# Performance work log

Hardware: AMD Instinct MI355X
Metric: run time of the kernel (lower is better)

The kernel has to match this reference:

```python
import jax, jax.numpy as jnp
import numpy as np

N, DIM, G, K = 100000, 512, 4, 16
GD = DIM // G
EPS = 1e-5

def _ln(x, g, b):
    mu = jnp.mean(x, axis=-1, keepdims=True)
    var = jnp.mean((x - mu) ** 2, axis=-1, keepdims=True)
    return (x - mu) / jnp.sqrt(var + EPS) * g + b

def setup_inputs() -> dict:
    key = jax.random.key(0)
    ks = jax.random.split(key, 12)
    s = 1.0 / np.sqrt(GD)
    return {
        "features": jax.random.normal(ks[0], (N, DIM), jnp.float32),
        "coords": jax.random.uniform(ks[1], (N, 3), jnp.float32),
        "neighbors": jax.random.randint(ks[2], (N, K), 0, N),
        "Wq": jax.random.normal(ks[3], (G, GD, GD), jnp.float32) * s,
        "Wk": jax.random.normal(ks[4], (G, GD, GD), jnp.float32) * s,
        "Wv": jax.random.normal(ks[5], (G, GD, GD), jnp.float32) * s,
        "Wo": jax.random.normal(ks[6], (DIM, DIM), jnp.float32) / np.sqrt(DIM),
        "bo": jnp.zeros((DIM,), jnp.float32),
        "ln1_g": jnp.ones((DIM,), jnp.float32),
        "ln1_b": jnp.zeros((DIM,), jnp.float32),
        "ln2_g": jnp.ones((DIM,), jnp.float32),
        "ln2_b": jnp.zeros((DIM,), jnp.float32),
        "W1": jax.random.normal(ks[7], (2 * DIM, DIM), jnp.float32) / np.sqrt(DIM),
        "b1": jnp.zeros((2 * DIM,), jnp.float32),
        "W2": jax.random.normal(ks[8], (DIM, 2 * DIM), jnp.float32) / np.sqrt(2 * DIM),
        "b2": jnp.zeros((DIM,), jnp.float32),
    }

def reference(features, coords, neighbors, Wq, Wk, Wv, Wo, bo, ln1_g, ln1_b, ln2_g, ln2_b, W1, b1, W2, b2):
    n = features.shape[0]
    residual = features
    x = _ln(features, ln1_g, ln1_b)
    xg = x.reshape(n, G, GD)                      # chunk along feature dim == group reshape
    # per-group Linear (no bias): y = x @ W.T with W (out,in)
    q = jnp.einsum('ngd,god->ngo', xg, Wq)
    k = jnp.einsum('ngd,god->ngo', xg, Wk)
    v = jnp.einsum('ngd,god->ngo', xg, Wv)
    nk = k[neighbors]                             # (N,K,G,GD) gather
    nv = v[neighbors]
    scale = jnp.asarray(1.0 / np.sqrt(GD), x.dtype)
    scores = jnp.einsum('ngd,nkgd->nkg', q, nk) * scale
    w = jax.nn.softmax(scores, axis=1)
    attn = jnp.einsum('nkg,nkgd->ngd', w, nv).reshape(n, DIM)
    out = attn @ Wo.T + bo + residual
    res2 = out
    y = _ln(out, ln2_g, ln2_b)
    y = jax.nn.gelu(y @ W1.T + b1, approximate=False) @ W2.T + b2
    return y + res2
```

## Files before the change

kernel.cpp:

```cpp
#include <hip/hip_runtime.h>
#include <hip/hip_bf16.h>
#include <math.h>

#define NPTS 100000
#define PAD_ROWS 100096
#define DIM 512
#define GRP 4
#define GD 128
#define K_NBR 16
#define EPS 1e-5f

using bf16x8 = __attribute__((ext_vector_type(8))) short;
using f32x4  = __attribute__((ext_vector_type(4))) float;
using short4v = __attribute__((ext_vector_type(4))) short;

__device__ inline float bf2f(short s) {
    unsigned u = ((unsigned)(unsigned short)s) << 16;
    union { unsigned u; float f; } c; c.u = u; return c.f;
}
__device__ inline short f2bf(float f) {
    union { float f; unsigned u; } c; c.f = f;
    unsigned u = c.u;
    unsigned r = (u + 0x7fffu + ((u >> 16) & 1u)) >> 16;
    return (short)r;
}

__device__ __forceinline__ void gload_lds16(short* lds, const short* g) {
    __builtin_amdgcn_global_load_lds(
        (const __attribute__((address_space(1))) unsigned int*)g,
        (__attribute__((address_space(3))) unsigned int*)lds, 16, 0, 0);
}

__global__ void cvt_kernel(const float* __restrict__ src, short* __restrict__ dst, int n) {
    int i = blockIdx.x * blockDim.x + threadIdx.x;
    int stride = gridDim.x * blockDim.x;
    for (; i < n; i += stride) dst[i] = f2bf(src[i]);
}

__global__ void prep_m_kernel(const float* __restrict__ wq, const float* __restrict__ wk,
                              short* __restrict__ mt) {
    int ge = blockIdx.x;
    int g = ge >> 7, e = ge & 127;
    int d = threadIdx.x;
    const float* Wq = wq + (size_t)g * GD * GD;
    const float* Wk = wk + (size_t)g * GD * GD;
    float acc = 0.0f;
    for (int o = 0; o < GD; ++o)
        acc += Wq[(size_t)o * GD + d] * Wk[(size_t)o * GD + e];
    mt[(size_t)ge * GD + d] = f2bf(acc * 0.08838834764831845f);
}

__global__ void prep_wov_kernel(const float* __restrict__ wo, const float* __restrict__ wv,
                                short* __restrict__ wov) {
    int o = blockIdx.x;
    int i = threadIdx.x;
    int g = i >> 7, i0 = i & 127;
    float acc = 0.0f;
    for (int d = 0; d < GD; ++d)
        acc += wo[(size_t)o * DIM + g * GD + d] * wv[((size_t)g * GD + d) * GD + i0];
    wov[(size_t)o * DIM + i] = f2bf(acc);
}

__global__ void ln_kernel(const float* __restrict__ in, const float* __restrict__ g,
                          const float* __restrict__ b, short* __restrict__ out) {
    int row = blockIdx.x;
    int tid = threadIdx.x;
    if (row >= NPTS) {
        short4v z; z[0] = 0; z[1] = 0; z[2] = 0; z[3] = 0;
        *(short4v*)(out + (size_t)row * DIM + tid * 4) = z;
        return;
    }
    const float4 x = *(const float4*)(in + (size_t)row * DIM + tid * 4);
    float s  = x.x + x.y + x.z + x.w;
    float sq = x.x * x.x + x.y * x.y + x.z * x.z + x.w * x.w;
    for (int m = 1; m < 64; m <<= 1) {
        s  += __shfl_xor(s, m);
        sq += __shfl_xor(sq, m);
    }
    __shared__ float ss[2], ssq[2];
    int wv = tid >> 6;
    if ((tid & 63) == 0) { ss[wv] = s; ssq[wv] = sq; }
    __syncthreads();
    s = ss[0] + ss[1]; sq = ssq[0] + ssq[1];
    float mu = s * (1.0f / DIM);
    float var = sq * (1.0f / DIM) - mu * mu;
    float rstd = rsqrtf(var + EPS);
    const float4 gg = *(const float4*)(g + tid * 4);
    const float4 bb = *(const float4*)(b + tid * 4);
    short4v o;
    o[0] = f2bf((x.x - mu) * rstd * gg.x + bb.x);
    o[1] = f2bf((x.y - mu) * rstd * gg.y + bb.y);
    o[2] = f2bf((x.z - mu) * rstd * gg.z + bb.z);
    o[3] = f2bf((x.w - mu) * rstd * gg.w + bb.w);
    *(short4v*)(out + (size_t)row * DIM + tid * 4) = o;
}

__device__ __forceinline__ void stage_tile(short* As, short* Bs,
        const short* aS, int as_, const short* bS, int bs_, int tid) {
    int ldRow = tid >> 2;
    int ldCol = (tid & 3) * 8;
    gload_lds16(As + (ldRow)      * 32 + ldCol, aS + (size_t)(ldRow)      * as_ + ldCol);
    gload_lds16(As + (ldRow + 64) * 32 + ldCol, aS + (size_t)(ldRow + 64) * as_ + ldCol);
    gload_lds16(Bs + (ldRow)      * 32 + ldCol, bS + (size_t)(ldRow)      * bs_ + ldCol);
    gload_lds16(Bs + (ldRow + 64) * 32 + ldCol, bS + (size_t)(ldRow + 64) * bs_ + ldCol);
}

__device__ __forceinline__ void compute_tile(const short* As, const short* Bs,
        int wr, int wc, int r, int ks, f32x4 (&acc)[4][4]) {
    bf16x8 a[4];
    #pragma unroll
    for (int m = 0; m < 4; ++m)
        a[m] = *(const bf16x8*)(As + (wr * 64 + m * 16 + r) * 32 + ks * 8);
    #pragma unroll
    for (int n = 0; n < 4; ++n) {
        bf16x8 b = *(const bf16x8*)(Bs + (wc * 64 + n * 16 + r) * 32 + ks * 8);
        #pragma unroll
        for (int m = 0; m < 4; ++m)
            acc[m][n] = __builtin_amdgcn_mfma_f32_16x16x32_bf16(a[m], b, acc[m][n], 0, 0, 0);
    }
}

template<int NK>
__device__ __forceinline__ void gemm_tile(
        const short* __restrict__ aBase, int as_,
        const short* __restrict__ bBase, int bs_,
        short* As0, short* Bs0, short* As1, short* Bs1, f32x4 (&acc)[4][4]) {
    int tid = threadIdx.x;
    int lane = tid & 63, wave = tid >> 6;
    int wr = wave >> 1, wc = wave & 1;
    int r = lane & 15, ks = lane >> 4;
    stage_tile(As0, Bs0, aBase, as_, bBase, bs_, tid);
    __syncthreads();
    #pragma unroll
    for (int kt = 0; kt < NK; kt += 2) {
        if (kt + 1 < NK)
            stage_tile(As1, Bs1, aBase + (kt + 1) * 32, as_, bBase + (kt + 1) * 32, bs_, tid);
        compute_tile(As0, Bs0, wr, wc, r, ks, acc);
        __syncthreads();
        if (kt + 2 < NK)
            stage_tile(As0, Bs0, aBase + (kt + 2) * 32, as_, bBase + (kt + 2) * 32, bs_, tid);
        compute_tile(As1, Bs1, wr, wc, r, ks, acc);
        __syncthreads();
    }
}

#define GEMM_LDS \
    __shared__ short As0[128 * 32], Bs0[128 * 32], As1[128 * 32], Bs1[128 * 32]

__global__ __launch_bounds__(256) void qproj_kernel(
        const short* __restrict__ x, const short* __restrict__ mt,
        short* __restrict__ qp) {
    GEMM_LDS;
    int nwg = gridDim.x;
    int bid = blockIdx.x;
    int tile = (bid & 7) * (nwg >> 3) + (bid >> 3);
    int rb = tile >> 2, g = tile & 3;
    int rowbase = rb * 128;
    int tid = threadIdx.x;
    int lane = tid & 63, wave = tid >> 6;
    int wr = wave >> 1, wc = wave & 1;
    int r = lane & 15, ks = lane >> 4;
    f32x4 acc[4][4];
    #pragma unroll
    for (int m = 0; m < 4; ++m)
        #pragma unroll
        for (int n = 0; n < 4; ++n)
            #pragma unroll
            for (int e = 0; e < 4; ++e) acc[m][n][e] = 0.0f;
    gemm_tile<4>(x + (size_t)rowbase * DIM + g * GD, DIM,
                 mt + (size_t)g * GD * GD, GD, As0, Bs0, As1, Bs1, acc);
    #pragma unroll
    for (int m = 0; m < 4; ++m)
        #pragma unroll
        for (int n = 0; n < 4; ++n)
            #pragma unroll
            for (int rr = 0; rr < 4; ++rr) {
                int orow = rowbase + wr * 64 + m * 16 + ks * 4 + rr;
                int lcol = wc * 64 + n * 16 + r;
                qp[(size_t)orow * DIM + g * GD + lcol] = f2bf(acc[m][n][rr]);
            }
}

__global__ __launch_bounds__(256) void attn_kernel(
        const short* __restrict__ qp, const short* __restrict__ x,
        const int* __restrict__ nbrs, short* __restrict__ t_out) {
    int b = blockIdx.x;
    int xcd = b & 7;
    int g = xcd >> 1;
    int quad = (b >> 3) * 2 + (xcd & 1);
    int tid = threadIdx.x;
    int wv = tid >> 6, lane = tid & 63;
    int n = quad * 4 + wv;
    int s = lane >> 4, t = lane & 15;
    int4 nbj = *(const int4*)(nbrs + (size_t)n * K_NBR + s * 4);
    int nbarr[4] = {nbj.x, nbj.y, nbj.z, nbj.w};
    size_t goff = (size_t)g * GD + t * 8;
    size_t qbase = (size_t)n * DIM + goff;
    bf16x8 qf = *(const bf16x8*)(qp + qbase);
    float qv[8];
    #pragma unroll
    for (int e = 0; e < 8; ++e) qv[e] = bf2f(qf[e]);
    bf16x8 xf[4];
    #pragma unroll
    for (int p = 0; p < 4; ++p)
        xf[p] = *(const bf16x8*)(x + (size_t)nbarr[p] * DIM + goff);
    float sc[4];
    #pragma unroll
    for (int p = 0; p < 4; ++p) {
        float dd = 0.0f;
        #pragma unroll
        for (int e = 0; e < 8; ++e) dd += qv[e] * bf2f(xf[p][e]);
        dd += __shfl_xor(dd, 1);
        dd += __shfl_xor(dd, 2);
        dd += __shfl_xor(dd, 4);
        dd += __shfl_xor(dd, 8);
        sc[p] = dd;
    }
    float mx = fmaxf(fmaxf(sc[0], sc[1]), fmaxf(sc[2], sc[3]));
    mx = fmaxf(mx, __shfl_xor(mx, 16));
    mx = fmaxf(mx, __shfl_xor(mx, 32));
    float ew[4]; float ssum = 0.0f;
    #pragma unroll
    for (int p = 0; p < 4; ++p) { ew[p] = __expf(sc[p] - mx); ssum += ew[p]; }
    ssum += __shfl_xor(ssum, 16);
    ssum += __shfl_xor(ssum, 32);
    float acc[8];
    #pragma unroll
    for (int d0 = 0; d0 < 8; ++d0) acc[d0] = 0.0f;
    #pragma unroll
    for (int p = 0; p < 4; ++p) {
        #pragma unroll
        for (int d0 = 0; d0 < 8; ++d0) acc[d0] += ew[p] * bf2f(xf[p][d0]);
    }
    #pragma unroll
    for (int d0 = 0; d0 < 8; ++d0) {
        acc[d0] += __shfl_xor(acc[d0], 16);
        acc[d0] += __shfl_xor(acc[d0], 32);
    }
    if (s == 0) {
        float inv = 1.0f / ssum;
        bf16x8 o;
        #pragma unroll
        for (int d0 = 0; d0 < 8; ++d0) o[d0] = f2bf(acc[d0] * inv);
        *(bf16x8*)(t_out + qbase) = o;
    }
}

__global__ __launch_bounds__(256) void outproj_kernel(
        const short* __restrict__ tbuf, const short* __restrict__ wov,
        const float* __restrict__ bo, const float* __restrict__ features,
        float* __restrict__ out) {
    GEMM_LDS;
    int nwg = gridDim.x;
    int bid = blockIdx.x;
    int tile = (bid & 7) * (nwg >> 3) + (bid >> 3);
    int rb = tile >> 2, cb = tile & 3;
    int rowbase = rb * 128, colbase = cb * 128;
    int tid = threadIdx.x;
    int lane = tid & 63, wave = tid >> 6;
    int wr = wave >> 1, wc = wave & 1;
    int r = lane & 15, ks = lane >> 4;
    f32x4 acc[4][4];
    #pragma unroll
    for (int m = 0; m < 4; ++m)
        #pragma unroll
        for (int n = 0; n < 4; ++n)
            #pragma unroll
            for (int e = 0; e < 4; ++e) acc[m][n][e] = 0.0f;
    gemm_tile<16>(tbuf + (size_t)rowbase * DIM, DIM,
                  wov + (size_t)colbase * DIM, DIM, As0, Bs0, As1, Bs1, acc);
    #pragma unroll
    for (int m = 0; m < 4; ++m)
        #pragma unroll
        for (int n = 0; n < 4; ++n)
            #pragma unroll
            for (int rr = 0; rr < 4; ++rr) {
                int orow = rowbase + wr * 64 + m * 16 + ks * 4 + rr;
                int ocol = colbase + wc * 64 + n * 16 + r;
                if (orow < NPTS) {
                    out[(size_t)orow * DIM + ocol] =
                        acc[m][n][rr] + bo[ocol] + features[(size_t)orow * DIM + ocol];
                }
            }
}

__global__ __launch_bounds__(256) void ffn1_kernel(
        const short* __restrict__ y, const short* __restrict__ w1,
        const float* __restrict__ b1, short* __restrict__ h) {
    GEMM_LDS;
    int nwg = gridDim.x;
    int bid = blockIdx.x;
    int tile = (bid & 7) * (nwg >> 3) + (bid >> 3);
    int rb = tile >> 3, cb = tile & 7;
    int rowbase = rb * 128, colbase = cb * 128;
    int tid = threadIdx.x;
    int lane = tid & 63, wave = tid >> 6;
    int wr = wave >> 1, wc = wave & 1;
    int r = lane & 15, ks = lane >> 4;
    f32x4 acc[4][4];
    #pragma unroll
    for (int m = 0; m < 4; ++m)
        #pragma unroll
        for (int n = 0; n < 4; ++n)
            #pragma unroll
            for (int e = 0; e < 4; ++e) acc[m][n][e] = 0.0f;
    gemm_tile<16>(y + (size_t)rowbase * DIM, DIM,
                  w1 + (size_t)colbase * DIM, DIM, As0, Bs0, As1, Bs1, acc);
    #pragma unroll
    for (int m = 0; m < 4; ++m)
        #pragma unroll
        for (int n = 0; n < 4; ++n)
            #pragma unroll
            for (int rr = 0; rr < 4; ++rr) {
                int orow = rowbase + wr * 64 + m * 16 + ks * 4 + rr;
                int ocol = colbase + wc * 64 + n * 16 + r;
                float xv = acc[m][n][rr] + b1[ocol];
                float xc = fminf(fmaxf(xv, -9.0f), 9.0f);
                float u = xc * (0.7978845608028654f + 0.0356774081f * xc * xc);
                float e2 = __expf(2.0f * u);
                float th = (e2 - 1.0f) / (e2 + 1.0f);
                float gl = 0.5f * xv * (1.0f + th);
                h[(size_t)orow * (2 * DIM) + ocol] = f2bf(gl);
            }
}

__global__ __launch_bounds__(256) void ffn2_kernel(
        const short* __restrict__ h, const short* __restrict__ w2,
        const float* __restrict__ b2, float* __restrict__ out) {
    GEMM_LDS;
    int nwg = gridDim.x;
    int bid = blockIdx.x;
    int tile = (bid & 7) * (nwg >> 3) + (bid >> 3);
    int rb = tile >> 2, cb = tile & 3;
    int rowbase = rb * 128, colbase = cb * 128;
    int tid = threadIdx.x;
    int lane = tid & 63, wave = tid >> 6;
    int wr = wave >> 1, wc = wave & 1;
    int r = lane & 15, ks = lane >> 4;
    f32x4 acc[4][4];
    #pragma unroll
    for (int m = 0; m < 4; ++m)
        #pragma unroll
        for (int n = 0; n < 4; ++n)
            #pragma unroll
            for (int e = 0; e < 4; ++e) acc[m][n][e] = 0.0f;
    gemm_tile<32>(h + (size_t)rowbase * (2 * DIM), 2 * DIM,
                  w2 + (size_t)colbase * (2 * DIM), 2 * DIM, As0, Bs0, As1, Bs1, acc);
    #pragma unroll
    for (int m = 0; m < 4; ++m)
        #pragma unroll
        for (int n = 0; n < 4; ++n)
            #pragma unroll
            for (int rr = 0; rr < 4; ++rr) {
                int orow = rowbase + wr * 64 + m * 16 + ks * 4 + rr;
                int ocol = colbase + wc * 64 + n * 16 + r;
                if (orow < NPTS) {
                    size_t idx = (size_t)orow * DIM + ocol;
                    out[idx] = acc[m][n][rr] + b2[ocol] + out[idx];
                }
            }
}

extern "C" void kernel_launch(void* const* d_in, const int* in_sizes, int n_in,
                              void* d_out, int out_size, void* d_ws, size_t ws_size,
                              hipStream_t stream) {
    const float* features = (const float*)d_in[0];
    const int*   neighbors = (const int*)d_in[2];
    const float* Wq = (const float*)d_in[3];
    const float* Wk = (const float*)d_in[4];
    const float* Wv = (const float*)d_in[5];
    const float* Wo = (const float*)d_in[6];
    const float* bo = (const float*)d_in[7];
    const float* ln1_g = (const float*)d_in[8];
    const float* ln1_b = (const float*)d_in[9];
    const float* ln2_g = (const float*)d_in[10];
    const float* ln2_b = (const float*)d_in[11];
    const float* W1 = (const float*)d_in[12];
    const float* b1 = (const float*)d_in[13];
    const float* W2 = (const float*)d_in[14];
    const float* b2 = (const float*)d_in[15];
    float* out = (float*)d_out;

    size_t slotElems = (size_t)PAD_ROWS * DIM;
    short* s0 = (short*)d_ws;
    short* s1 = s0 + slotElems;
    short* s2 = s1 + slotElems;
    short* mt_b  = s2 + slotElems;
    short* wov_b = mt_b + GRP * GD * GD;
    short* w1_b  = wov_b + DIM * DIM;
    short* w2_b  = w1_b + 2 * DIM * DIM;

    cvt_kernel<<<256, 256, 0, stream>>>(W1, w1_b, 2 * DIM * DIM);
    cvt_kernel<<<256, 256, 0, stream>>>(W2, w2_b, 2 * DIM * DIM);
    prep_m_kernel<<<GRP * GD, GD, 0, stream>>>(Wq, Wk, mt_b);
    prep_wov_kernel<<<DIM, DIM, 0, stream>>>(Wo, Wv, wov_b);

    ln_kernel<<<PAD_ROWS, 128, 0, stream>>>(features, ln1_g, ln1_b, s0);

    qproj_kernel<<<(PAD_ROWS / 128) * 4, 256, 0, stream>>>(s0, mt_b, s1);

    attn_kernel<<<NPTS, 256, 0, stream>>>(s1, s0, neighbors, s2);

    outproj_kernel<<<(PAD_ROWS / 128) * 4, 256, 0, stream>>>(s2, wov_b, bo, features, out);

    ln_kernel<<<PAD_ROWS, 128, 0, stream>>>(out, ln2_g, ln2_b, s0);

    ffn1_kernel<<<(PAD_ROWS / 128) * 8, 256, 0, stream>>>(s0, w1_b, b1, s1);

    ffn2_kernel<<<(PAD_ROWS / 128) * 4, 256, 0, stream>>>(s1, w2_b, b2, out);
}
```

Baseline: 1.125 ms.

## Use 256x256x64 GEMM tiles with 8 waves and remainder-aware XCD block mapping

Replaces the 128x128x32, 4-wave GEMM tiling in the out-projection and both FFN kernels with a 256x256 output tile, K-step 64, 512 threads and double-buffered LDS. Each wave computes a 128x64 sub-tile with 8x4 MFMA accumulators. The larger tile raises arithmetic intensity and cuts global and LDS traffic per FLOP, but uses 128KB of LDS per block and many more accumulator registers, which limits occupancy. It also adds an XCD block remap that handles grid sizes not divisible by 8.

```diff
diff --git a/kernel.cpp b/kernel.cpp
--- a/kernel.cpp
+++ b/kernel.cpp
@@ -29,6 +29,13 @@
     __builtin_amdgcn_global_load_lds(
         (const __attribute__((address_space(1))) unsigned int*)g,
         (__attribute__((address_space(3))) unsigned int*)lds, 16, 0, 0);
+}
+
+__device__ __forceinline__ int xcd_map(int bid, int nwg) {
+    int q = nwg >> 3, r8 = nwg & 7;
+    int xcd = bid & 7, idx = bid >> 3;
+    int base = (xcd < r8) ? xcd * (q + 1) : r8 * (q + 1) + (xcd - r8) * q;
+    return base + idx;
 }
 
 __global__ void cvt_kernel(const float* __restrict__ src, short* __restrict__ dst, int n) {
@@ -95,6 +102,74 @@
     *(short4v*)(out + (size_t)row * DIM + tid * 4) = o;
 }
 
+#define TSZ (256 * 64)
+
+__device__ __forceinline__ void stage256(short* As, short* Bs,
+        const short* aS, int as_, const short* bS, int bs_, int tid) {
+    int ldRow = tid >> 3;
+    int ldCol = (tid & 7) * 8;
+    #pragma unroll
+    for (int i = 0; i < 4; ++i) {
+        gload_lds16(As + (ldRow + i * 64) * 64 + ldCol, aS + (size_t)(ldRow + i * 64) * as_ + ldCol);
+        gload_lds16(Bs + (ldRow + i * 64) * 64 + ldCol, bS + (size_t)(ldRow + i * 64) * bs_ + ldCol);
+    }
+}
+
+__device__ __forceinline__ void compute256(const short* As, const short* Bs,
+        int wr, int wc, int r, int ks, f32x4 (&acc)[8][4]) {
+    #pragma unroll
+    for (int ks2 = 0; ks2 < 2; ++ks2) {
+        bf16x8 a[8];
+        #pragma unroll
+        for (int m = 0; m < 8; ++m)
+            a[m] = *(const bf16x8*)(As + (wr * 128 + m * 16 + r) * 64 + ks2 * 32 + ks * 8);
+        #pragma unroll
+        for (int n = 0; n < 4; ++n) {
+            bf16x8 b = *(const bf16x8*)(Bs + (wc * 64 + n * 16 + r) * 64 + ks2 * 32 + ks * 8);
+            #pragma unroll
+            for (int m = 0; m < 8; ++m)
+                acc[m][n] = __builtin_amdgcn_mfma_f32_16x16x32_bf16(a[m], b, acc[m][n], 0, 0, 0);
+        }
+    }
+}
+
+template<int NT>
+__device__ __forceinline__ void gemm256(
+        const short* __restrict__ aBase, int as_,
+        const short* __restrict__ bBase, int bs_,
+        short* As, short* Bs, f32x4 (&acc)[8][4]) {
+    int tid = threadIdx.x;
+    int lane = tid & 63, wave = tid >> 6;
+    int wr = wave >> 2, wc = wave & 3;
+    int r = lane & 15, ks = lane >> 4;
+    stage256(As, Bs, aBase, as_, bBase, bs_, tid);
+    __syncthreads();
+    for (int kt = 0; kt < NT; kt += 2) {
+        if (kt + 1 < NT)
+            stage256(As + TSZ, Bs + TSZ, aBase + (kt + 1) * 64, as_, bBase + (kt + 1) * 64, bs_, tid);
+        compute256(As, Bs, wr, wc, r, ks, acc);
+        __syncthreads();
+        if (kt + 2 < NT)
+            stage256(As, Bs, aBase + (kt + 2) * 64, as_, bBase + (kt + 2) * 64, bs_, tid);
+        compute256(As + TSZ, Bs + TSZ, wr, wc, r, ks, acc);
+        __syncthreads();
+    }
+}
+
+#define GEMM256_PRE \
+    __shared__ short As[2 * TSZ], Bs[2 * TSZ]; \
+    int tid = threadIdx.x; \
+    int lane = tid & 63, wave = tid >> 6; \
+    int wr = wave >> 2, wc = wave & 3; \
+    int r = lane & 15, ks = lane >> 4; \
+    f32x4 acc[8][4]; \
+    _Pragma("unroll") \
+    for (int m = 0; m < 8; ++m) \
+        _Pragma("unroll") \
+        for (int n = 0; n < 4; ++n) \
+            _Pragma("unroll") \
+            for (int e = 0; e < 4; ++e) acc[m][n][e] = 0.0f;
+
 __device__ __forceinline__ void stage_tile(short* As, short* Bs,
         const short* aS, int as_, const short* bS, int bs_, int tid) {
     int ldRow = tid >> 2;
@@ -144,16 +219,13 @@
     }
 }
 
-#define GEMM_LDS \
-    __shared__ short As0[128 * 32], Bs0[128 * 32], As1[128 * 32], Bs1[128 * 32]
-
 __global__ __launch_bounds__(256) void qproj_kernel(
         const short* __restrict__ x, const short* __restrict__ mt,
         short* __restrict__ qp) {
-    GEMM_LDS;
+    __shared__ short As0[128 * 32], Bs0[128 * 32], As1[128 * 32], Bs1[128 * 32];
     int nwg = gridDim.x;
     int bid = blockIdx.x;
-    int tile = (bid & 7) * (nwg >> 3) + (bid >> 3);
+    int tile = xcd_map(bid, nwg);
     int rb = tile >> 2, g = tile & 3;
     int rowbase = rb * 128;
     int tid = threadIdx.x;
@@ -246,36 +318,23 @@
     }
 }
 
-__global__ __launch_bounds__(256) void outproj_kernel(
+__global__ __launch_bounds__(512, 2) void outproj_kernel(
         const short* __restrict__ tbuf, const short* __restrict__ wov,
         const float* __restrict__ bo, const float* __restrict__ features,
         float* __restrict__ out) {
-    GEMM_LDS;
-    int nwg = gridDim.x;
-    int bid = blockIdx.x;
-    int tile = (bid & 7) * (nwg >> 3) + (bid >> 3);
-    int rb = tile >> 2, cb = tile & 3;
-    int rowbase = rb * 128, colbase = cb * 128;
-    int tid = threadIdx.x;
-    int lane = tid & 63, wave = tid >> 6;
-    int wr = wave >> 1, wc = wave & 1;
-    int r = lane & 15, ks = lane >> 4;
-    f32x4 acc[4][4];
-    #pragma unroll
-    for (int m = 0; m < 4; ++m)
+    GEMM256_PRE;
+    int tile = xcd_map(blockIdx.x, gridDim.x);
+    int rt = tile >> 1, ct = tile & 1;
+    int rowbase = rt * 256, colbase = ct * 256;
+    gemm256<8>(tbuf + (size_t)rowbase * DIM, DIM,
+               wov + (size_t)colbase * DIM, DIM, As, Bs, acc);
+    #pragma unroll
+    for (int m = 0; m < 8; ++m)
         #pragma unroll
         for (int n = 0; n < 4; ++n)
             #pragma unroll
-            for (int e = 0; e < 4; ++e) acc[m][n][e] = 0.0f;
-    gemm_tile<16>(tbuf + (size_t)rowbase * DIM, DIM,
-                  wov + (size_t)colbase * DIM, DIM, As0, Bs0, As1, Bs1, acc);
-    #pragma unroll
-    for (int m = 0; m < 4; ++m)
-        #pragma unroll
-        for (int n = 0; n < 4; ++n)
-            #pragma unroll
             for (int rr = 0; rr < 4; ++rr) {
-                int orow = rowbase + wr * 64 + m * 16 + ks * 4 + rr;
+                int orow = rowbase + wr * 128 + m * 16 + ks * 4 + rr;
                 int ocol = colbase + wc * 64 + n * 16 + r;
                 if (orow < NPTS) {
                     out[(size_t)orow * DIM + ocol] =
@@ -284,35 +343,22 @@
             }
 }
 
-__global__ __launch_bounds__(256) void ffn1_kernel(
+__global__ __launch_bounds__(512, 2) void ffn1_kernel(
         const short* __restrict__ y, const short* __restrict__ w1,
         const float* __restrict__ b1, short* __restrict__ h) {
-    GEMM_LDS;
-    int nwg = gridDim.x;
-    int bid = blockIdx.x;
-    int tile = (bid & 7) * (nwg >> 3) + (bid >> 3);
-    int rb = tile >> 3, cb = tile & 7;
-    int rowbase = rb * 128, colbase = cb * 128;
-    int tid = threadIdx.x;
-    int lane = tid & 63, wave = tid >> 6;
-    int wr = wave >> 1, wc = wave & 1;
-    int r = lane & 15, ks = lane >> 4;
-    f32x4 acc[4][4];
-    #pragma unroll
-    for (int m = 0; m < 4; ++m)
+    GEMM256_PRE;
+    int tile = xcd_map(blockIdx.x, gridDim.x);
+    int rt = tile >> 2, ct = tile & 3;
+    int rowbase = rt * 256, colbase = ct * 256;
+    gemm256<8>(y + (size_t)rowbase * DIM, DIM,
+               w1 + (size_t)colbase * DIM, DIM, As, Bs, acc);
+    #pragma unroll
+    for (int m = 0; m < 8; ++m)
         #pragma unroll
         for (int n = 0; n < 4; ++n)
             #pragma unroll
-            for (int e = 0; e < 4; ++e) acc[m][n][e] = 0.0f;
-    gemm_tile<16>(y + (size_t)rowbase * DIM, DIM,
-                  w1 + (size_t)colbase * DIM, DIM, As0, Bs0, As1, Bs1, acc);
-    #pragma unroll
-    for (int m = 0; m < 4; ++m)
-        #pragma unroll
-        for (int n = 0; n < 4; ++n)
-            #pragma unroll
             for (int rr = 0; rr < 4; ++rr) {
-                int orow = rowbase + wr * 64 + m * 16 + ks * 4 + rr;
+                int orow = rowbase + wr * 128 + m * 16 + ks * 4 + rr;
                 int ocol = colbase + wc * 64 + n * 16 + r;
                 float xv = acc[m][n][rr] + b1[ocol];
                 float xc = fminf(fmaxf(xv, -9.0f), 9.0f);
@@ -324,35 +370,22 @@
             }
 }
 
-__global__ __launch_bounds__(256) void ffn2_kernel(
+__global__ __launch_bounds__(512, 2) void ffn2_kernel(
         const short* __restrict__ h, const short* __restrict__ w2,
         const float* __restrict__ b2, float* __restrict__ out) {
-    GEMM_LDS;
-    int nwg = gridDim.x;
-    int bid = blockIdx.x;
-    int tile = (bid & 7) * (nwg >> 3) + (bid >> 3);
-    int rb = tile >> 2, cb = tile & 3;
-    int rowbase = rb * 128, colbase = cb * 128;
-    int tid = threadIdx.x;
-    int lane = tid & 63, wave = tid >> 6;
-    int wr = wave >> 1, wc = wave & 1;
-    int r = lane & 15, ks = lane >> 4;
-    f32x4 acc[4][4];
-    #pragma unroll
-    for (int m = 0; m < 4; ++m)
+    GEMM256_PRE;
+    int tile = xcd_map(blockIdx.x, gridDim.x);
+    int rt = tile >> 1, ct = tile & 1;
+    int rowbase = rt * 256, colbase = ct * 256;
+    gemm256<16>(h + (size_t)rowbase * (2 * DIM), 2 * DIM,
+                w2 + (size_t)colbase * (2 * DIM), 2 * DIM, As, Bs, acc);
+    #pragma unroll
+    for (int m = 0; m < 8; ++m)
         #pragma unroll
         for (int n = 0; n < 4; ++n)
             #pragma unroll
-            for (int e = 0; e < 4; ++e) acc[m][n][e] = 0.0f;
-    gemm_tile<32>(h + (size_t)rowbase * (2 * DIM), 2 * DIM,
-                  w2 + (size_t)colbase * (2 * DIM), 2 * DIM, As0, Bs0, As1, Bs1, acc);
-    #pragma unroll
-    for (int m = 0; m < 4; ++m)
-        #pragma unroll
-        for (int n = 0; n < 4; ++n)
-            #pragma unroll
             for (int rr = 0; rr < 4; ++rr) {
-                int orow = rowbase + wr * 64 + m * 16 + ks * 4 + rr;
+                int orow = rowbase + wr * 128 + m * 16 + ks * 4 + rr;
                 int ocol = colbase + wc * 64 + n * 16 + r;
                 if (orow < NPTS) {
                     size_t idx = (size_t)orow * DIM + ocol;
@@ -401,11 +434,11 @@
 
     attn_kernel<<<NPTS, 256, 0, stream>>>(s1, s0, neighbors, s2);
 
-    outproj_kernel<<<(PAD_ROWS / 128) * 4, 256, 0, stream>>>(s2, wov_b, bo, features, out);
+    outproj_kernel<<<(PAD_ROWS / 256) * 2, 512, 0, stream>>>(s2, wov_b, bo, features, out);
 
     ln_kernel<<<PAD_ROWS, 128, 0, stream>>>(out, ln2_g, ln2_b, s0);
 
-    ffn1_kernel<<<(PAD_ROWS / 128) * 8, 256, 0, stream>>>(s0, w1_b, b1, s1);
-
-    ffn2_kernel<<<(PAD_ROWS / 128) * 4, 256, 0, stream>>>(s1, w2_b, b2, out);
-}
+    ffn1_kernel<<<(PAD_ROWS / 256) * 4, 512, 0, stream>>>(s0, w1_b, b1, s1);
+
+    ffn2_kernel<<<(PAD_ROWS / 256) * 2, 512, 0, stream>>>(s1, w2_b, b2, out);
+}
```

Result: slower. 1.579 ms (+40.3%).
